# Optimization experiments

Measured on AMD Instinct MI355X. Metric: run time of the kernel, lower is better.

Reference implementation:

```python
import jax, jax.numpy as jnp
import numpy as np

N_NODES = 100000


def gat_conv(x, edge_index, W, att_src, att_dst, bias, concat=True, negative_slope=0.2):
    """PyG-style GATConv (eval mode, dropout off, self-loops added)."""
    N = x.shape[0]
    H, C = att_src.shape
    # add self loops (PyG default add_self_loops=True)
    ar = jnp.arange(N, dtype=edge_index.dtype)
    ei = jnp.concatenate([edge_index, jnp.stack([ar, ar])], axis=1)
    src, dst = ei[0], ei[1]

    h = (x @ W).reshape(N, H, C)                       # [N,H,C]
    a_src = (h * att_src[None]).sum(-1)                # [N,H]
    a_dst = (h * att_dst[None]).sum(-1)                # [N,H]

    e = jax.nn.leaky_relu(a_src[src] + a_dst[dst], negative_slope)  # [E,H]
    # segment softmax over destination nodes
    e_max = jax.ops.segment_max(e, dst, num_segments=N)            # [N,H]
    ex = jnp.exp(e - jax.lax.stop_gradient(e_max)[dst])
    denom = jax.ops.segment_sum(ex, dst, num_segments=N)           # [N,H]
    alpha = ex / (denom[dst] + 1e-16)                              # [E,H]

    out = jax.ops.segment_sum(alpha[:, :, None] * h[src], dst, num_segments=N)  # [N,H,C]
    out = out.reshape(N, H * C) if concat else out.mean(axis=1)
    return out + bias


def setup_inputs() -> dict:
    key = jax.random.key(0)
    ks = jax.random.split(key, 9)
    N, E, F_in, H, C = N_NODES, 3200000, 16, 4, 8
    x = jax.random.normal(ks[0], (N, F_in), dtype=jnp.float32)
    edge_index = jax.random.randint(ks[1], (2, E), 0, N, dtype=jnp.int64)
    s1 = 1.0 / np.sqrt(F_in)
    s2 = 1.0 / np.sqrt(H * C)
    return {
        "x": x,
        "edge_index": edge_index,
        "W1": jax.random.normal(ks[2], (F_in, H * C), dtype=jnp.float32) * s1,
        "att_src1": jax.random.normal(ks[3], (H, C), dtype=jnp.float32) * s2,
        "att_dst1": jax.random.normal(ks[4], (H, C), dtype=jnp.float32) * s2,
        "b1": jnp.zeros((H * C,), dtype=jnp.float32),
        "W2": jax.random.normal(ks[5], (H * C, 1), dtype=jnp.float32) * s2,
        "att_src2": jax.random.normal(ks[6], (1, 1), dtype=jnp.float32),
        "att_dst2": jax.random.normal(ks[7], (1, 1), dtype=jnp.float32),
        "b2": jnp.zeros((1,), dtype=jnp.float32),
    }


def reference(x, edge_index, W1, att_src1, att_dst1, b1, W2, att_src2, att_dst2, b2):
    h = jax.nn.elu(gat_conv(x, edge_index, W1, att_src1, att_dst1, b1, concat=True))
    return gat_conv(h, edge_index, W2, att_src2, att_dst2, b2, concat=False)
```

## Files before the change

kernel.cpp:

```cpp
#include <hip/hip_runtime.h>

#define LRELU_SLOPE 0.2f
#define BN 64
#define BSH 6
#define NC 2048
#define CAP 3840
#define TILE 16384

__device__ __forceinline__ float lrelu(float x) { return x > 0.f ? x : LRELU_SLOPE * x; }
__device__ __forceinline__ float eexp(float x)  { return __expf(fminf(x, 80.f)); }

__device__ __forceinline__ unsigned short f2bf(float f) {
    unsigned u = __float_as_uint(f);
    u += 0x7FFF + ((u >> 16) & 1);
    return (unsigned short)(u >> 16);
}
__device__ __forceinline__ float bf2f(unsigned short h) {
    return __uint_as_float((unsigned)h << 16);
}

__global__ __launch_bounds__(256) void kA(
    const float* __restrict__ x, const float* __restrict__ W1,
    const float* __restrict__ att_src1, const float* __restrict__ att_dst1,
    unsigned short* __restrict__ h1, unsigned short* __restrict__ as1,
    float* __restrict__ ad1,
    const int* __restrict__ dst, int* __restrict__ hist, int* __restrict__ bukcnt,
    int N, int E, int nbn)
{
    __shared__ float sW[512];
    __shared__ float sAs[32], sAd[32];
    __shared__ int hl[NC];
    int tid = threadIdx.x;

    if ((int)blockIdx.x >= nbn) {
        int blk = blockIdx.x - nbn;
        for (int i = tid; i < NC; i += 256) hl[i] = 0;
        __syncthreads();
        int e0 = blk * TILE, e1 = min(e0 + TILE, E);
        for (int e = e0 + tid; e < e1; e += 256)
            atomicAdd(&hl[dst[e] >> BSH], 1);
        __syncthreads();
        for (int i = tid; i < NC; i += 256) {
            int v = hl[i];
            hist[(size_t)blk * NC + i] = v;
            if (v) atomicAdd(bukcnt + i, v);
        }
        return;
    }

    for (int i = tid; i < 512; i += 256) sW[i] = W1[i];
    if (tid < 32) { sAs[tid] = att_src1[tid]; sAd[tid] = att_dst1[tid]; }
    __syncthreads();
    int n = blockIdx.x * 256 + tid;
    if (n >= N) return;

    float xr[16];
    const float4* xp = (const float4*)(x + (size_t)n * 16);
    float4 v0 = xp[0], v1 = xp[1], v2 = xp[2], v3 = xp[3];
    xr[0]=v0.x; xr[1]=v0.y; xr[2]=v0.z;  xr[3]=v0.w;
    xr[4]=v1.x; xr[5]=v1.y; xr[6]=v1.z;  xr[7]=v1.w;
    xr[8]=v2.x; xr[9]=v2.y; xr[10]=v2.z; xr[11]=v2.w;
    xr[12]=v3.x;xr[13]=v3.y;xr[14]=v3.z; xr[15]=v3.w;

    float h[32];
#pragma unroll
    for (int j = 0; j < 32; ++j) {
        float acc = 0.f;
#pragma unroll
        for (int i = 0; i < 16; ++i) acc = fmaf(xr[i], sW[i * 32 + j], acc);
        h[j] = acc;
    }

    float asr[4], adr[4];
#pragma unroll
    for (int hh = 0; hh < 4; ++hh) {
        float as = 0.f, ad = 0.f;
#pragma unroll
        for (int c = 0; c < 8; ++c) {
            as = fmaf(h[hh * 8 + c], sAs[hh * 8 + c], as);
            ad = fmaf(h[hh * 8 + c], sAd[hh * 8 + c], ad);
        }
        asr[hh] = as; adr[hh] = ad;
    }

    ushort4* h1p = (ushort4*)(h1 + (size_t)n * 32);
#pragma unroll
    for (int j = 0; j < 32; j += 4) {
        ushort4 q;
        q.x = f2bf(h[j]); q.y = f2bf(h[j+1]); q.z = f2bf(h[j+2]); q.w = f2bf(h[j+3]);
        h1p[j >> 2] = q;
    }
    ushort4 aq;
    aq.x = f2bf(asr[0]); aq.y = f2bf(asr[1]); aq.z = f2bf(asr[2]); aq.w = f2bf(asr[3]);
    *(ushort4*)(as1 + (size_t)n * 4) = aq;
    *(float4*)(ad1 + (size_t)n * 4) = make_float4(adr[0], adr[1], adr[2], adr[3]);
}

__global__ __launch_bounds__(256) void kscan(
    int* __restrict__ hist, const int* __restrict__ bukcnt,
    int* __restrict__ bukoff, int NBLK)
{
    __shared__ int sd[256];
    int tid = threadIdx.x;
    if ((int)blockIdx.x == NC) {
        int4 a = ((const int4*)bukcnt)[2 * tid];
        int4 c = ((const int4*)bukcnt)[2 * tid + 1];
        int tsum = a.x + a.y + a.z + a.w + c.x + c.y + c.z + c.w;
        sd[tid] = tsum; __syncthreads();
        for (int off = 1; off < 256; off <<= 1) {
            int t = (tid >= off) ? sd[tid - off] : 0; __syncthreads();
            sd[tid] += t; __syncthreads();
        }
        int excl = sd[tid] - tsum;
        int4 oa, ob;
        oa.x = excl;        oa.y = oa.x + a.x; oa.z = oa.y + a.y; oa.w = oa.z + a.z;
        ob.x = oa.w + a.w;  ob.y = ob.x + c.x; ob.z = ob.y + c.y; ob.w = ob.z + c.z;
        ((int4*)bukoff)[2 * tid] = oa;
        ((int4*)bukoff)[2 * tid + 1] = ob;
        return;
    }
    int b = blockIdx.x;
    int carry = 0;
    for (int base = 0; base < NBLK; base += 256) {
        int idx = base + tid;
        int v = (idx < NBLK) ? hist[(size_t)idx * NC + b] : 0;
        sd[tid] = v; __syncthreads();
        for (int off = 1; off < 256; off <<= 1) {
            int t = (tid >= off) ? sd[tid - off] : 0; __syncthreads();
            sd[tid] += t; __syncthreads();
        }
        int incl = sd[tid];
        int tot  = sd[255];
        if (idx < NBLK) hist[(size_t)idx * NC + b] = carry + incl - v;
        carry += tot;
        __syncthreads();
    }
}

__global__ __launch_bounds__(1024) void kpass2(
    const int* __restrict__ src, const int* __restrict__ dst,
    const int* __restrict__ hist, const int* __restrict__ bukoff,
    unsigned* __restrict__ ebuk, int E)
{
    __shared__ int cur[NC];
    int tid = threadIdx.x, blk = blockIdx.x;
    cur[tid] = bukoff[tid] + hist[(size_t)blk * NC + tid];
    cur[tid + 1024] = bukoff[tid + 1024] + hist[(size_t)blk * NC + tid + 1024];
    __syncthreads();
    int e0 = blk * TILE, e1 = min(e0 + TILE, E);
    for (int e = e0 + tid; e < e1; e += 1024) {
        int s = src[e], d = dst[e];
        int b = d >> BSH;
        int pos = atomicAdd(&cur[b], 1);
        ebuk[pos] = ((unsigned)(d & (BN - 1)) << 17) | (unsigned)s;
    }
}

__global__ __launch_bounds__(256, 6) void ksort_agg1(
    unsigned* __restrict__ ebuk, const int* __restrict__ bukoff,
    const unsigned short* __restrict__ h1, const unsigned short* __restrict__ as1,
    const float* __restrict__ ad1,
    const float* __restrict__ b1, const float* __restrict__ W2,
    float* __restrict__ h2, int* __restrict__ rowptr, int N)
{
    __shared__ int sbuf[CAP];
    __shared__ int cnt[BN], exc[BN], cur[BN];
    __shared__ float sb[32], sw[32];
    int tid = threadIdx.x;
    int b = blockIdx.x;
    int n0 = b << BSH;
    int r0 = bukoff[b], r1 = bukoff[b + 1];
    int tot = r1 - r0;

    if (tid < 32) { sb[tid] = b1[tid]; sw[tid] = W2[tid]; }
    if (tid < BN) cnt[tid] = 0;
    __syncthreads();

    for (int i = tid; i < tot; i += 256)
        atomicAdd(&cnt[ebuk[r0 + i] >> 17], 1);
    __syncthreads();

    if (tid < BN) exc[tid] = cnt[tid];
    __syncthreads();
    for (int off = 1; off < BN; off <<= 1) {
        int t = 0;
        if (tid < BN && tid >= off) t = exc[tid - off];
        __syncthreads();
        if (tid < BN) exc[tid] += t;
        __syncthreads();
    }
    if (tid < BN) {
        int e = exc[tid] - cnt[tid];
        exc[tid] = e;
        cur[tid] = e;
        int n = n0 + tid;
        if (n <= N) rowptr[n] = r0 + e;
    }
    __syncthreads();

    for (int i = tid; i < tot; i += 256) {
        unsigned pk = ebuk[r0 + i];
        int dl = pk >> 17;
        int pos = atomicAdd(&cur[dl], 1);
        if (pos < CAP) sbuf[pos] = (int)(pk & 0x1FFFF);
    }
    __syncthreads();
    for (int i = tid; i < tot; i += 256)
        ebuk[r0 + i] = (unsigned)sbuf[min(i, CAP - 1)];

    int g = tid >> 3, l = tid & 7;
    int hsel = l >> 1, c0 = l * 4;
    for (int base = 0; base < BN; base += 32) {
        int dl = base + g;
        int n = n0 + dl;
        if (n < N) {
            float adh = ad1[(size_t)n * 4 + hsel];
            float ass = bf2f(as1[(size_t)n * 4 + hsel]);
            float wself = eexp(lrelu(ass + adh));
            ushort4 hu = *(const ushort4*)(h1 + (size_t)n * 32 + c0);
            float dsum = wself;
            float4 acc = make_float4(wself * bf2f(hu.x), wself * bf2f(hu.y),
                                     wself * bf2f(hu.z), wself * bf2f(hu.w));
            int p0 = exc[dl];
            int p1 = min(p0 + cnt[dl], CAP);
            int p = p0;
            for (; p + 8 <= p1; p += 8) {
                int sidx[8];
                float av[8];
                ushort4 uv[8];
#pragma unroll
                for (int q = 0; q < 8; ++q) sidx[q] = sbuf[p + q];
#pragma unroll
                for (int q = 0; q < 8; ++q) {
                    av[q] = bf2f(as1[(size_t)sidx[q] * 4 + hsel]);
                    uv[q] = *(const ushort4*)(h1 + (size_t)sidx[q] * 32 + c0);
                }
#pragma unroll
                for (int q = 0; q < 8; ++q) {
                    float w = eexp(lrelu(av[q] + adh));
                    dsum += w;
                    acc.x = fmaf(w, bf2f(uv[q].x), acc.x);
                    acc.y = fmaf(w, bf2f(uv[q].y), acc.y);
                    acc.z = fmaf(w, bf2f(uv[q].z), acc.z);
                    acc.w = fmaf(w, bf2f(uv[q].w), acc.w);
                }
            }
            for (; p < p1; ++p) {
                int s = sbuf[p];
                float ash = bf2f(as1[(size_t)s * 4 + hsel]);
                ushort4 hs = *(const ushort4*)(h1 + (size_t)s * 32 + c0);
                float w = eexp(lrelu(ash + adh));
                dsum += w;
                acc.x = fmaf(w, bf2f(hs.x), acc.x);
                acc.y = fmaf(w, bf2f(hs.y), acc.y);
                acc.z = fmaf(w, bf2f(hs.z), acc.z);
                acc.w = fmaf(w, bf2f(hs.w), acc.w);
            }
            float inv = 1.f / (dsum + 1e-16f);
            float4 bb = *(const float4*)(sb + c0);
            float4 ww = *(const float4*)(sw + c0);
            float partial = 0.f, o;
            o = fmaf(acc.x, inv, bb.x); o = o > 0.f ? o : __expf(o) - 1.f; partial = fmaf(o, ww.x, partial);
            o = fmaf(acc.y, inv, bb.y); o = o > 0.f ? o : __expf(o) - 1.f; partial = fmaf(o, ww.y, partial);
            o = fmaf(acc.z, inv, bb.z); o = o > 0.f ? o : __expf(o) - 1.f; partial = fmaf(o, ww.z, partial);
            o = fmaf(acc.w, inv, bb.w); o = o > 0.f ? o : __expf(o) - 1.f; partial = fmaf(o, ww.w, partial);
            partial += __shfl_xor(partial, 1);
            partial += __shfl_xor(partial, 2);
            partial += __shfl_xor(partial, 4);
            if (l == 0) h2[n] = partial;
        }
    }
}

__global__ __launch_bounds__(256) void kagg2(
    const unsigned* __restrict__ esrc, const int* __restrict__ rowptr,
    const float* __restrict__ h2,
    const float* __restrict__ att_src2, const float* __restrict__ att_dst2,
    const float* __restrict__ b2, float* __restrict__ out, int N)
{
    int tid = threadIdx.x;
    int g = tid >> 3, l = tid & 7;
    int n = blockIdx.x * 32 + g;
    if (n >= N) return;
    float s2 = att_src2[0], d2 = att_dst2[0];
    int r0 = rowptr[n], r1 = rowptr[n + 1];
    float h2d = h2[n];
    float add = h2d * d2;
    float den = 0.f, acc = 0.f;
    if (l == 0) {
        float ws = eexp(lrelu(fmaf(h2d, s2, add)));
        den = ws; acc = ws * h2d;
    }
    for (int p = r0 + l; p < r1; p += 8) {
        int s = (int)esrc[p];
        float hs = h2[s];
        float w = eexp(lrelu(fmaf(hs, s2, add)));
        den += w;
        acc = fmaf(w, hs, acc);
    }
    den += __shfl_xor(den, 1); acc += __shfl_xor(acc, 1);
    den += __shfl_xor(den, 2); acc += __shfl_xor(acc, 2);
    den += __shfl_xor(den, 4); acc += __shfl_xor(acc, 4);
    if (l == 0) out[n] = acc / (den + 1e-16f) + b2[0];
}

extern "C" void kernel_launch(void* const* d_in, const int* in_sizes, int n_in,
                              void* d_out, int out_size, void* d_ws, size_t ws_size,
                              hipStream_t stream)
{
    const float* x        = (const float*)d_in[0];
    const int*   ei       = (const int*)d_in[1];
    const float* W1       = (const float*)d_in[2];
    const float* att_src1 = (const float*)d_in[3];
    const float* att_dst1 = (const float*)d_in[4];
    const float* b1       = (const float*)d_in[5];
    const float* W2       = (const float*)d_in[6];
    const float* att_src2 = (const float*)d_in[7];
    const float* att_dst2 = (const float*)d_in[8];
    const float* b2       = (const float*)d_in[9];

    const int N = in_sizes[0] / 16;
    const int E = in_sizes[1] / 2;
    const int* src = ei;
    const int* dst = ei + E;

    const int NBUK = (N + BN - 1) >> BSH;
    const int NBLK = (E + TILE - 1) / TILE;
    const int nb_n = (N + 255) / 256;

    unsigned short* h1  = (unsigned short*)d_ws;
    unsigned short* as1 = h1 + (size_t)N * 32;
    float* ad1   = (float*)(as1 + (size_t)N * 4);
    float* h2    = ad1 + (size_t)N * 4;
    int* rowptr  = (int*)(h2 + N);
    int* bukcnt  = rowptr + N + 64;
    int* bukoff  = bukcnt + NC;
    int* hist    = bukoff + NC;
    unsigned* ebuk = (unsigned*)(hist + (size_t)NBLK * NC);

    hipMemsetAsync(bukcnt, 0, NC * sizeof(int), stream);

    kA<<<nb_n + NBLK, 256, 0, stream>>>(x, W1, att_src1, att_dst1,
                                        h1, as1, ad1, dst, hist, bukcnt,
                                        N, E, nb_n);
    kscan<<<NC + 1, 256, 0, stream>>>(hist, bukcnt, bukoff, NBLK);
    kpass2<<<NBLK, 1024, 0, stream>>>(src, dst, hist, bukoff, ebuk, E);
    ksort_agg1<<<NBUK, 256, 0, stream>>>(ebuk, bukoff, h1, as1, ad1,
                                         b1, W2, h2, rowptr, N);
    kagg2<<<(N + 31) / 32, 256, 0, stream>>>(ebuk, rowptr, h2,
                                             att_src2, att_dst2,
                                             b2, (float*)d_out, N);
}
```

Measured before the change: 227.0 us.

## Stage bucketed edges in shared memory before writing contiguous runs to global

The scatter pass now builds a per-tile local bucket layout in LDS, using an in-block prefix scan of the tile histogram, and then copies each bucket's run to its global offset. This replaces random per-edge global writes with more contiguous ones. The tile size is halved so the staging buffer fits in LDS, which doubles the number of tiles and the histogram and scan work. The per-bucket copy loop is serial per thread, so it may write poorly coalesced memory and leave load imbalanced.

```diff
diff --git a/kernel.cpp b/kernel.cpp
--- a/kernel.cpp
+++ b/kernel.cpp
@@ -5,7 +5,7 @@
 #define BSH 6
 #define NC 2048
 #define CAP 3840
-#define TILE 16384
+#define TILE 8192
 
 __device__ __forceinline__ float lrelu(float x) { return x > 0.f ? x : LRELU_SLOPE * x; }
 __device__ __forceinline__ float eexp(float x)  { return __expf(fminf(x, 80.f)); }
@@ -97,8 +97,8 @@
 }
 
 __global__ __launch_bounds__(256) void kscan(
-    int* __restrict__ hist, const int* __restrict__ bukcnt,
-    int* __restrict__ bukoff, int NBLK)
+    const int* __restrict__ hist, int* __restrict__ histoff,
+    const int* __restrict__ bukcnt, int* __restrict__ bukoff, int NBLK)
 {
     __shared__ int sd[256];
     int tid = threadIdx.x;
@@ -131,28 +131,54 @@
         }
         int incl = sd[tid];
         int tot  = sd[255];
-        if (idx < NBLK) hist[(size_t)idx * NC + b] = carry + incl - v;
+        if (idx < NBLK) histoff[(size_t)idx * NC + b] = carry + incl - v;
         carry += tot;
         __syncthreads();
     }
 }
 
-__global__ __launch_bounds__(1024) void kpass2(
+__global__ __launch_bounds__(512) void kpass2(
     const int* __restrict__ src, const int* __restrict__ dst,
-    const int* __restrict__ hist, const int* __restrict__ bukoff,
+    const int* __restrict__ hist, const int* __restrict__ histoff,
+    const int* __restrict__ bukoff,
     unsigned* __restrict__ ebuk, int E)
 {
+    __shared__ unsigned staged[TILE];
+    __shared__ int bstart[NC + 1];
     __shared__ int cur[NC];
+    __shared__ int partial[512];
     int tid = threadIdx.x, blk = blockIdx.x;
-    cur[tid] = bukoff[tid] + hist[(size_t)blk * NC + tid];
-    cur[tid + 1024] = bukoff[tid + 1024] + hist[(size_t)blk * NC + tid + 1024];
-    __syncthreads();
+
+    int4 c = ((const int4*)(hist + (size_t)blk * NC))[tid];
+    int tsum = c.x + c.y + c.z + c.w;
+    partial[tid] = tsum;
+    __syncthreads();
+    for (int off = 1; off < 512; off <<= 1) {
+        int t = (tid >= off) ? partial[tid - off] : 0; __syncthreads();
+        partial[tid] += t; __syncthreads();
+    }
+    int excl = partial[tid] - tsum;
+    int b4 = tid * 4;
+    int e0v = excl, e1v = excl + c.x, e2v = e1v + c.y, e3v = e2v + c.z;
+    bstart[b4] = e0v; bstart[b4+1] = e1v; bstart[b4+2] = e2v; bstart[b4+3] = e3v;
+    cur[b4] = e0v; cur[b4+1] = e1v; cur[b4+2] = e2v; cur[b4+3] = e3v;
+    if (tid == 511) bstart[NC] = e3v + c.w;
+    __syncthreads();
+
     int e0 = blk * TILE, e1 = min(e0 + TILE, E);
-    for (int e = e0 + tid; e < e1; e += 1024) {
+    for (int e = e0 + tid; e < e1; e += 512) {
         int s = src[e], d = dst[e];
         int b = d >> BSH;
         int pos = atomicAdd(&cur[b], 1);
-        ebuk[pos] = ((unsigned)(d & (BN - 1)) << 17) | (unsigned)s;
+        staged[pos] = ((unsigned)(d & (BN - 1)) << 17) | (unsigned)s;
+    }
+    __syncthreads();
+
+    for (int b = tid; b < NC; b += 512) {
+        int p0 = bstart[b], p1 = bstart[b + 1];
+        int gb = bukoff[b] + histoff[(size_t)blk * NC + b];
+        for (int p = p0; p < p1; ++p)
+            ebuk[gb + (p - p0)] = staged[p];
     }
 }
 
@@ -336,15 +362,16 @@
     int* bukcnt  = rowptr + N + 64;
     int* bukoff  = bukcnt + NC;
     int* hist    = bukoff + NC;
-    unsigned* ebuk = (unsigned*)(hist + (size_t)NBLK * NC);
+    int* histoff = hist + (size_t)NBLK * NC;
+    unsigned* ebuk = (unsigned*)(histoff + (size_t)NBLK * NC);
 
     hipMemsetAsync(bukcnt, 0, NC * sizeof(int), stream);
 
     kA<<<nb_n + NBLK, 256, 0, stream>>>(x, W1, att_src1, att_dst1,
                                         h1, as1, ad1, dst, hist, bukcnt,
                                         N, E, nb_n);
-    kscan<<<NC + 1, 256, 0, stream>>>(hist, bukcnt, bukoff, NBLK);
-    kpass2<<<NBLK, 1024, 0, stream>>>(src, dst, hist, bukoff, ebuk, E);
+    kscan<<<NC + 1, 256, 0, stream>>>(hist, histoff, bukcnt, bukoff, NBLK);
+    kpass2<<<NBLK, 512, 0, stream>>>(src, dst, hist, histoff, bukoff, ebuk, E);
     ksort_agg1<<<NBUK, 256, 0, stream>>>(ebuk, bukoff, h1, as1, ad1,
                                          b1, W2, h2, rowptr, N);
     kagg2<<<(N + 31) / 32, 256, 0, stream>>>(ebuk, rowptr, h2,
```

New measurement: 222.0 us. 1.02x faster.
